# Optimization experiments

Measured on AMD Instinct MI355X. Metric: run time of the kernel, lower is better.

## Reference

```python
import jax, jax.numpy as jnp
import numpy as np

S = 28
B = 2
C = 20
D = 28  # max((B-1)*(4+C)+4, 4*B+C)
LAMBDA_COORD = 2.0
LAMBDA_CE = 1.0
BATCH = 512


def setup_inputs() -> dict:
    key = jax.random.key(0)
    k1, k2 = jax.random.split(key)
    preds = jax.random.normal(k1, (BATCH, S, S, D), dtype=jnp.float32)
    targets = jax.random.normal(k2, (BATCH, S, S, D), dtype=jnp.float32)
    return {"preds": preds, "targets": targets}


def reference(preds, targets):
    batch = preds.shape[0]
    # Box slices: bb*(4+C) : bb*(4+C)+4 for each of B boxes (stride 4+C, as in source)
    box_idx = (jnp.arange(B)[:, None] * (4 + C) + jnp.arange(4)[None, :]).reshape(-1)  # [B*4]
    p_box = preds[..., box_idx]    # [batch,S,S,B*4]
    t_box = targets[..., box_idx]
    coord_loss = LAMBDA_COORD * jnp.sum((p_box - t_box) ** 2)

    # Classification: cells where target class slice sums > 0 get CE vs argmax label
    pred_cls = preds[..., 4 * B:4 * B + C]    # [batch,S,S,C]
    tgt_cls = targets[..., 4 * B:4 * B + C]
    mask = jnp.sum(tgt_cls, axis=-1) > 0                      # [batch,S,S]
    labels = jnp.argmax(tgt_cls, axis=-1)                     # [batch,S,S]
    logp = jax.nn.log_softmax(pred_cls, axis=-1)
    ce = -jnp.take_along_axis(logp, labels[..., None], axis=-1)[..., 0]
    ce_loss = LAMBDA_CE * jnp.sum(jnp.where(mask, ce, 0.0))

    return (coord_loss + ce_loss) / batch
```

## Files before the change

### kernel.cpp

```cpp
#include <hip/hip_runtime.h>

#define S_DIM 28
#define B_BOX 2
#define C_CLS 20
#define D_CH 28
#define BATCH_N 512
#define CELLS (BATCH_N * S_DIM * S_DIM)
#define BLOCK 256
#define NBLOCKS (CELLS / BLOCK)


__global__ __launch_bounds__(BLOCK) void yolo_cell_kernel(
    const float* __restrict__ preds,
    const float* __restrict__ tgts,
    float* __restrict__ partial)
{
    const int cell = blockIdx.x * BLOCK + threadIdx.x;
    const float4* p4 = reinterpret_cast<const float4*>(preds + (size_t)cell * D_CH);
    const float4* t4 = reinterpret_cast<const float4*>(tgts  + (size_t)cell * D_CH);

    float p[D_CH], t[D_CH];
    #pragma unroll
    for (int i = 0; i < 7; ++i) {
        float4 a = p4[i];
        p[4*i+0] = a.x; p[4*i+1] = a.y; p[4*i+2] = a.z; p[4*i+3] = a.w;
    }
    #pragma unroll
    for (int i = 0; i < 7; ++i) {
        float4 b = t4[i];
        t[4*i+0] = b.x; t[4*i+1] = b.y; t[4*i+2] = b.z; t[4*i+3] = b.w;
    }

    float coord = 0.0f;
    #pragma unroll
    for (int j = 0; j < 4; ++j) {
        float d0 = p[j]      - t[j];      coord = fmaf(d0, d0, coord);
        float d1 = p[24 + j] - t[24 + j]; coord = fmaf(d1, d1, coord);
    }

    float m    = -INFINITY;
    float tsum = 0.0f;
    float tmax = -INFINITY;
    int   lab  = 0;
    #pragma unroll
    for (int j = 0; j < C_CLS; ++j) {
        float pc = p[8 + j];
        float tc = t[8 + j];
        m = fmaxf(m, pc);
        tsum += tc;
        if (tc > tmax) { tmax = tc; lab = j; }
    }
    float se = 0.0f;
    #pragma unroll
    for (int j = 0; j < C_CLS; ++j) se += __expf(p[8 + j] - m);
    float plab = p[8];
    #pragma unroll
    for (int j = 1; j < C_CLS; ++j) plab = (lab == j) ? p[8 + j] : plab;
    float ce = -(plab - m - __logf(se));

    float loss = 2.0f * coord + ((tsum > 0.0f) ? ce : 0.0f);

    #pragma unroll
    for (int off = 32; off > 0; off >>= 1) loss += __shfl_down(loss, off, 64);

    __shared__ float sm[BLOCK / 64];
    const int wid  = threadIdx.x >> 6;
    const int lane = threadIdx.x & 63;
    if (lane == 0) sm[wid] = loss;
    __syncthreads();
    if (threadIdx.x == 0) {
        float s = 0.0f;
        #pragma unroll
        for (int w = 0; w < BLOCK / 64; ++w) s += sm[w];
        partial[blockIdx.x] = s;
    }
}

__global__ __launch_bounds__(BLOCK) void yolo_final_kernel(
    const float* __restrict__ partial,
    float* __restrict__ out)
{
    float s = 0.0f;
    for (int i = threadIdx.x; i < NBLOCKS; i += BLOCK) s += partial[i];
    #pragma unroll
    for (int off = 32; off > 0; off >>= 1) s += __shfl_down(s, off, 64);

    __shared__ float sm[BLOCK / 64];
    const int wid  = threadIdx.x >> 6;
    const int lane = threadIdx.x & 63;
    if (lane == 0) sm[wid] = s;
    __syncthreads();
    if (threadIdx.x == 0) {
        float tot = 0.0f;
        #pragma unroll
        for (int w = 0; w < BLOCK / 64; ++w) tot += sm[w];
        out[0] = tot * (1.0f / (float)BATCH_N);
    }
}

extern "C" void kernel_launch(void* const* d_in, const int* in_sizes, int n_in,
                              void* d_out, int out_size, void* d_ws, size_t ws_size,
                              hipStream_t stream)
{
    const float* preds = (const float*)d_in[0];
    const float* tgts  = (const float*)d_in[1];
    float* out     = (float*)d_out;
    float* partial = (float*)d_ws;

    yolo_cell_kernel<<<NBLOCKS, BLOCK, 0, stream>>>(preds, tgts, partial);
    yolo_final_kernel<<<1, BLOCK, 0, stream>>>(partial, out);
}
```

Before: 107.1 us.

## Coalesce loads via swizzled LDS transpose and fuse final reduction with atomics

Each block now loads its 256 cells' data with fully coalesced float4 reads, stages them in shared memory with an XOR swizzle to avoid bank conflicts, then each thread reads its own cell. The separate final reduction kernel is removed; each block atomically adds its scaled partial sum into a zeroed output. This targets poorly coalesced strided global loads and a second launch, at the cost of 64KB of LDS per block limiting occupancy, plus a memset and non-deterministic summation order.

```diff
diff --git a/kernel.cpp b/kernel.cpp
--- a/kernel.cpp
+++ b/kernel.cpp
@@ -1,34 +1,52 @@
 #include <hip/hip_runtime.h>
 
-#define S_DIM 28
-#define B_BOX 2
 #define C_CLS 20
 #define D_CH 28
 #define BATCH_N 512
-#define CELLS (BATCH_N * S_DIM * S_DIM)
+#define CELLS (BATCH_N * 28 * 28)
 #define BLOCK 256
-#define NBLOCKS (CELLS / BLOCK)
+#define CPB 256
+#define NBLOCKS (CELLS / CPB)
 
 
-__global__ __launch_bounds__(BLOCK) void yolo_cell_kernel(
+__global__ __launch_bounds__(BLOCK) void yolo_fused_kernel(
     const float* __restrict__ preds,
     const float* __restrict__ tgts,
-    float* __restrict__ partial)
+    float* __restrict__ out)
 {
-    const int cell = blockIdx.x * BLOCK + threadIdx.x;
-    const float4* p4 = reinterpret_cast<const float4*>(preds + (size_t)cell * D_CH);
-    const float4* t4 = reinterpret_cast<const float4*>(tgts  + (size_t)cell * D_CH);
+    __shared__ float ldsP[CPB * 32];
+    __shared__ float ldsT[CPB * 32];
+
+    const int tid = threadIdx.x;
+    const size_t base = (size_t)blockIdx.x * (CPB * D_CH);
+    const float4* gp = reinterpret_cast<const float4*>(preds + base);
+    const float4* gt = reinterpret_cast<const float4*>(tgts + base);
+
+    float4 vp[7], vt[7];
+    #pragma unroll
+    for (int k = 0; k < 7; ++k) vp[k] = gp[tid + BLOCK * k];
+    #pragma unroll
+    for (int k = 0; k < 7; ++k) vt[k] = gt[tid + BLOCK * k];
+
+    #pragma unroll
+    for (int k = 0; k < 7; ++k) {
+        const int idx  = tid + BLOCK * k;
+        const int cell = idx / 7;
+        const int c4   = idx - cell * 7;
+        const int slot = c4 ^ (cell & 7);
+        *reinterpret_cast<float4*>(&ldsP[cell * 32 + slot * 4]) = vp[k];
+        *reinterpret_cast<float4*>(&ldsT[cell * 32 + slot * 4]) = vt[k];
+    }
+    __syncthreads();
 
     float p[D_CH], t[D_CH];
     #pragma unroll
-    for (int i = 0; i < 7; ++i) {
-        float4 a = p4[i];
-        p[4*i+0] = a.x; p[4*i+1] = a.y; p[4*i+2] = a.z; p[4*i+3] = a.w;
-    }
-    #pragma unroll
-    for (int i = 0; i < 7; ++i) {
-        float4 b = t4[i];
-        t[4*i+0] = b.x; t[4*i+1] = b.y; t[4*i+2] = b.z; t[4*i+3] = b.w;
+    for (int c4 = 0; c4 < 7; ++c4) {
+        const int slot = c4 ^ (tid & 7);
+        float4 a = *reinterpret_cast<const float4*>(&ldsP[tid * 32 + slot * 4]);
+        float4 b = *reinterpret_cast<const float4*>(&ldsT[tid * 32 + slot * 4]);
+        p[4*c4+0] = a.x; p[4*c4+1] = a.y; p[4*c4+2] = a.z; p[4*c4+3] = a.w;
+        t[4*c4+0] = b.x; t[4*c4+1] = b.y; t[4*c4+2] = b.z; t[4*c4+3] = b.w;
     }
 
     float coord = 0.0f;
@@ -64,37 +82,13 @@
     for (int off = 32; off > 0; off >>= 1) loss += __shfl_down(loss, off, 64);
 
     __shared__ float sm[BLOCK / 64];
-    const int wid  = threadIdx.x >> 6;
-    const int lane = threadIdx.x & 63;
+    const int wid  = tid >> 6;
+    const int lane = tid & 63;
     if (lane == 0) sm[wid] = loss;
     __syncthreads();
-    if (threadIdx.x == 0) {
-        float s = 0.0f;
-        #pragma unroll
-        for (int w = 0; w < BLOCK / 64; ++w) s += sm[w];
-        partial[blockIdx.x] = s;
-    }
-}
-
-__global__ __launch_bounds__(BLOCK) void yolo_final_kernel(
-    const float* __restrict__ partial,
-    float* __restrict__ out)
-{
-    float s = 0.0f;
-    for (int i = threadIdx.x; i < NBLOCKS; i += BLOCK) s += partial[i];
-    #pragma unroll
-    for (int off = 32; off > 0; off >>= 1) s += __shfl_down(s, off, 64);
-
-    __shared__ float sm[BLOCK / 64];
-    const int wid  = threadIdx.x >> 6;
-    const int lane = threadIdx.x & 63;
-    if (lane == 0) sm[wid] = s;
-    __syncthreads();
-    if (threadIdx.x == 0) {
-        float tot = 0.0f;
-        #pragma unroll
-        for (int w = 0; w < BLOCK / 64; ++w) tot += sm[w];
-        out[0] = tot * (1.0f / (float)BATCH_N);
+    if (tid == 0) {
+        float s = sm[0] + sm[1] + sm[2] + sm[3];
+        atomicAdd(out, s * (1.0f / (float)BATCH_N));
     }
 }
 
@@ -104,9 +98,8 @@
 {
     const float* preds = (const float*)d_in[0];
     const float* tgts  = (const float*)d_in[1];
-    float* out     = (float*)d_out;
-    float* partial = (float*)d_ws;
+    float* out = (float*)d_out;
 
-    yolo_cell_kernel<<<NBLOCKS, BLOCK, 0, stream>>>(preds, tgts, partial);
-    yolo_final_kernel<<<1, BLOCK, 0, stream>>>(partial, out);
+    hipMemsetAsync(out, 0, (size_t)out_size * sizeof(float), stream);
+    yolo_fused_kernel<<<NBLOCKS, BLOCK, 0, stream>>>(preds, tgts, out);
 }
```

Result: slower. 115.1 us (+7.4%).
